# Kernel optimization log

Measured on AMD Instinct MI355X. Metric: run time of the kernel, lower is better.

## Reference

```python
import jax, jax.numpy as jnp
import numpy as np

P1 = np.array([[1000.0, 0.0, 128.0, 64000.0],
               [0.0, 1000.0, 128.0, 64000.0],
               [0.0, 0.0, 1.0, 500.0]])
P2 = np.array([[-128.0, 0.0, 1000.0, 64000.0],
               [-128.0, 1000.0, 0.0, 64000.0],
               [-1.0, 0.0, 0.0, 500.0]])


def calculate_fundamental_matrix(P_src, P_dst):
    # l2 = F21 @ x1 : maps a point in P_src onto a line in P_dst
    C1 = -np.linalg.inv(P_src[:3, :3]) @ P_src[:3, 3]
    e = P_dst @ np.append(C1, 1.0)          # epipole of src camera center in dst view
    return np.cross(e, np.eye(3) * -1) @ P_dst @ np.linalg.pinv(P_src)


def setup_inputs() -> dict:
    key = jax.random.key(0)
    view1 = jax.random.normal(key, (8, 4, 256, 256), dtype=jnp.float32)
    F21 = calculate_fundamental_matrix(P1, P2).astype(np.float32)
    return {"view1": view1, "F": jnp.asarray(F21)}


def reference(view1, F):
    """Epipolar image translation: out(x2) = line integral of view1 along the
    epipolar line l1 = F^T @ x2 (bilinear sampling in v, unit steps in u,
    zero outside the image). Matches fume_torch_lib.translate semantics."""
    B, C, H, W = view1.shape
    dt = view1.dtype
    F = F.astype(dt)
    ys = jnp.arange(H, dtype=dt)[:, None]   # (H,1)
    xs = jnp.arange(W, dtype=dt)[None, :]   # (1,W)
    # line coefficients l = F^T @ [x, y, 1], per output pixel -> (H,W)
    a = F[0, 0] * xs + F[1, 0] * ys + F[2, 0]
    b = F[0, 1] * xs + F[1, 1] * ys + F[2, 1]
    c = F[0, 2] * xs + F[1, 2] * ys + F[2, 2]
    n = jnp.sqrt(a * a + b * b) + jnp.asarray(1e-12, dt)
    a, b, c = a / n, b / n, c / n
    ok = (jnp.abs(b) > 1e-6).astype(dt)                 # drop near-vertical lines
    b_safe = jnp.where(jnp.abs(b) > 1e-6, b, jnp.asarray(1.0, dt))

    def step(acc, u):
        uf = u.astype(dt)
        v = -(a * uf + c) / b_safe                      # (H,W) source row per out pixel
        v0 = jnp.floor(v)
        f = v - v0
        i0 = v0.astype(jnp.int32)
        i1 = i0 + 1
        m0 = ((i0 >= 0) & (i0 < H)).astype(dt)
        m1 = ((i1 >= 0) & (i1 < H)).astype(dt)
        col = jax.lax.dynamic_index_in_dim(view1, u, axis=3, keepdims=False)  # (B,C,H)
        s0 = col[:, :, jnp.clip(i0, 0, H - 1)]          # (B,C,H,W)
        s1 = col[:, :, jnp.clip(i1, 0, H - 1)]
        val = (s0 * (1.0 - f) * m0 + s1 * f * m1) * ok
        return acc + val, None

    out, _ = jax.lax.scan(step, jnp.zeros_like(view1), jnp.arange(W))
    return out
```

## Files before the change

kernel.cpp:

```cpp
#include <hip/hip_runtime.h>
#include <cstdint>

constexpr int Hh = 256, Ww = 256, BCc = 32;
constexpr int RBLK = 35;
constexpr int USTRIDE = RBLK * BCc * 8 * 2;
constexpr int UPLANES = 264;

typedef _Float16 half2v   __attribute__((ext_vector_type(2)));
typedef _Float16 half8v   __attribute__((ext_vector_type(8)));
typedef __fp16   fp16x2   __attribute__((ext_vector_type(2)));
typedef float    float16v __attribute__((ext_vector_type(16)));
typedef uint32_t uint4v   __attribute__((ext_vector_type(4)));

static __device__ inline half2v pack2(float a, float b) {
    fp16x2 r = __builtin_amdgcn_cvt_pkrtz(a, b);
    return __builtin_bit_cast(half2v, r);
}

__global__ __launch_bounds__(256) void fume_pack(const float* __restrict__ in,
                                                 char* __restrict__ T4) {
    const int t   = threadIdx.x;
    const int bid = blockIdx.x;
    if (bid >= 512) {
        constexpr int NA = UPLANES * 3 * 32;
        constexpr int NB = 8 * 32 * 32;
        for (int id = (bid - 512) * 256 + t; id < NA + NB; id += 8 * 256) {
            int u, blk, ch;
            if (id < NA) {
                u = id / 96;
                int rem = id - u * 96;
                int bsel = rem >> 5;
                blk = (bsel == 0) ? 0 : (bsel == 1 ? 33 : 34);
                ch = rem & 31;
            } else {
                int id2 = id - NA;
                u = 256 + (id2 >> 10);
                int rem = id2 & 1023;
                blk = 1 + (rem >> 5);
                ch = rem & 31;
            }
            uint4v z = {0, 0, 0, 0};
            *(uint4v*)(T4 + (size_t)u * USTRIDE + blk * 512 + ch * 16) = z;
        }
        return;
    }
    __shared__ float lds[8][8][65];
    const int chg = bid & 3;
    const int r0  = ((bid >> 2) & 31) * 8;
    const int u0  = (bid >> 7) * 64;
    const int blk = (r0 >> 3) + 1;

#pragma unroll
    for (int it = 0; it < 16; ++it) {
        int idx = it * 256 + t;
        int ch = idx >> 9, rr = (idx >> 6) & 7, uu = idx & 63;
        lds[ch][rr][uu] =
            in[(chg * 8 + ch) * (Hh * Ww) + (r0 + rr) * Ww + u0 + uu];
    }
    __syncthreads();
    const int chl = t & 7;
#pragma unroll
    for (int p = 0; p < 2; ++p) {
        int u_l = (t >> 3) + p * 32;
        uint32_t w[4];
#pragma unroll
        for (int j = 0; j < 4; ++j) {
            half2v pr = pack2(lds[chl][2 * j][u_l], lds[chl][2 * j + 1][u_l]);
            __builtin_memcpy(&w[j], &pr, 4);
        }
        uint4v val = {w[0], w[1], w[2], w[3]};
        *(uint4v*)(T4 + (size_t)(u0 + u_l) * USTRIDE + blk * 512
                   + (chg * 8 + chl) * 16) = val;
    }
}

__global__ __launch_bounds__(256, 4) void fume_mfma(const char* __restrict__ T4,
                                                    const float* __restrict__ Fm,
                                                    float* __restrict__ out) {
    __shared__ float red[4][32][33];
    const int t    = threadIdx.x;
    const int lane = t & 63;
    const int wq   = t >> 6;
    const int px   = lane & 31;
    const int h    = lane >> 5;
    const int x0   = ((int)blockIdx.x & 7) * 32;
    const int y    = (int)blockIdx.x >> 3;
    const int x    = x0 + px;

    float xf = (float)x, yf = (float)y;
    float a = Fm[0] * xf + Fm[3] * yf + Fm[6];
    float b = Fm[1] * xf + Fm[4] * yf + Fm[7];
    float c = Fm[2] * xf + Fm[5] * yf + Fm[8];
    float n = sqrtf(a * a + b * b) + 1e-12f;
    a /= n; b /= n; c /= n;

    float alpha, beta_i;
    int u_lo, u_hi;
    if (fabsf(b) > 1e-6f) {
        alpha  = -a / b;
        beta_i = -c / b + 8.f;
        u_lo = 0; u_hi = Ww - 1;
        if (fabsf(alpha) > 1e-12f) {
            float inv = 1.f / alpha;
            float t0 = (7.f - beta_i) * inv;
            float t1 = (264.f - beta_i) * inv;
            int lo = (int)floorf(fminf(t0, t1));
            int hi = (int)ceilf (fmaxf(t0, t1));
            u_lo = lo > 0 ? lo : 0;
            u_hi = hi < (Ww - 1) ? hi : (Ww - 1);
        } else if (beta_i <= 7.f || beta_i >= 264.f) {
            u_lo = 1 << 20; u_hi = -(1 << 20);
        }
    } else {
        alpha = 0.f; beta_i = 3.0e4f;
        u_lo = 1 << 20; u_hi = -(1 << 20);
    }

    float xA = (float)x0, xB = (float)(x0 + 31);
    float aA = Fm[0] * xA + Fm[3] * yf + Fm[6];
    float bA = Fm[1] * xA + Fm[4] * yf + Fm[7];
    float cA = Fm[2] * xA + Fm[5] * yf + Fm[8];
    float aB = Fm[0] * xB + Fm[3] * yf + Fm[6];
    float bB = Fm[1] * xB + Fm[4] * yf + Fm[7];
    float cB = Fm[2] * xB + Fm[5] * yf + Fm[8];
    float alA = -aA / bA, beA = -cA / bA + 8.f;
    float alB = -aB / bB, beB = -cB / bB + 8.f;

    int lo = u_lo, hi = u_hi;
#pragma unroll
    for (int off = 1; off < 64; off <<= 1) {
        int l2 = __shfl_xor(lo, off, 64);
        int h2 = __shfl_xor(hi, off, 64);
        lo = lo < l2 ? lo : l2;
        hi = hi > h2 ? hi : h2;
    }
    lo = __builtin_amdgcn_readfirstlane(lo);
    hi = __builtin_amdgcn_readfirstlane(hi);

    float16v acc = {0.f, 0.f, 0.f, 0.f, 0.f, 0.f, 0.f, 0.f,
                    0.f, 0.f, 0.f, 0.f, 0.f, 0.f, 0.f, 0.f};

    if (lo <= hi) {
        int len = hi - lo + 1;
        int C   = (len + 3) >> 2;
        int cq  = (C + 3) >> 2;
        int nit = C - wq * cq;
        nit = nit < 0 ? 0 : (nit > cq ? cq : nit);
        int us  = lo + wq * cq * 4;

        float uf  = (float)(us + lane);
        float vAl = fmaf(alA, uf, beA);
        float vBl = fmaf(alB, uf, beB);
        float mnu = fminf(vAl, vBl);
        float Mf  = floorf(fmaf(mnu, 0.125f, -0.125f));
        Mf = fmaxf(0.f, fminf(Mf, 33.f));
        int   vMo  = (int)Mf << 9;
        float vB8f = Mf * 8.f;
        int   vB8i = __builtin_bit_cast(int, vB8f);

        float v   = fmaf(alpha, (float)us, beta_i);
        float l8h = (float)(8 * h);
        const char* pb  = T4 + (size_t)us * USTRIDE;
        const int voff  = (h << 9) + (px << 4);

        const half2v one2  = {(_Float16)1.f, (_Float16)1.f};
        const half2v zero2 = {(_Float16)0.f, (_Float16)0.f};

        uint4v bA4[4], bB4[4], bC4[4];

#define FUME_ISS(BUF, BASE)                                                   \
    do {                                                                      \
        _Pragma("unroll")                                                     \
        for (int i_ = 0; i_ < 4; ++i_) {                                      \
            int idx_ = (BASE) + i_;                                           \
            int Mo_  = __builtin_amdgcn_readlane(vMo, idx_);                  \
            (BUF)[i_] = *(const uint4v*)(pb + (size_t)idx_ * USTRIDE          \
                                         + (size_t)Mo_ + voff);               \
        }                                                                     \
    } while (0)

#define FUME_COMP(BUF, BASE)                                                  \
    do {                                                                      \
        _Pragma("unroll")                                                     \
        for (int i_ = 0; i_ < 4; ++i_) {                                      \
            int idx_ = (BASE) + i_;                                           \
            float b8_ = __builtin_bit_cast(                                   \
                float, __builtin_amdgcn_readlane(vB8i, idx_));                \
            float vbl_ = (v - b8_) - l8h;                                     \
            half2v vb2_ = pack2(vbl_, vbl_);                                  \
            uint32_t aw_[4];                                                  \
            _Pragma("unroll")                                                 \
            for (int j_ = 0; j_ < 4; ++j_) {                                  \
                half2v cj_ = {(_Float16)(float)(2 * j_),                      \
                              (_Float16)(float)(2 * j_ + 1)};                 \
                half2v d_  = vb2_ - cj_;                                      \
                half2v ad_ = __builtin_elementwise_abs(d_);                   \
                half2v tj_ = __builtin_elementwise_max(one2 - ad_, zero2);    \
                __builtin_memcpy(&aw_[j_], &tj_, 4);                          \
            }                                                                 \
            half8v A_;                                                        \
            __builtin_memcpy(&A_, aw_, 16);                                   \
            half8v B_ = __builtin_bit_cast(half8v, (BUF)[i_]);                \
            acc = __builtin_amdgcn_mfma_f32_32x32x16_f16(A_, B_, acc, 0, 0, 0);\
            v += alpha;                                                       \
        }                                                                     \
    } while (0)

        if (nit > 0) {
            FUME_ISS(bA4, 0);
            if (nit > 1) FUME_ISS(bB4, 4);
            int cc = 0;
            for (;;) {
                if (cc + 2 < nit) FUME_ISS(bC4, (cc + 2) * 4);
                FUME_COMP(bA4, cc * 4);
                if (++cc >= nit) break;
                if (cc + 2 < nit) FUME_ISS(bA4, (cc + 2) * 4);
                FUME_COMP(bB4, cc * 4);
                if (++cc >= nit) break;
                if (cc + 2 < nit) FUME_ISS(bB4, (cc + 2) * 4);
                FUME_COMP(bC4, cc * 4);
                if (++cc >= nit) break;
            }
        }
#undef FUME_ISS
#undef FUME_COMP
    }

#pragma unroll
    for (int r = 0; r < 16; ++r) {
        int m = (r & 3) + 8 * (r >> 2) + 4 * h;
        red[wq][m][px] = acc[r];
    }
    __syncthreads();
    {
        int pxs = t & 31, cg = t >> 5;
#pragma unroll
        for (int jj = 0; jj < 4; ++jj) {
            int ch = cg + 8 * jj;
            float val = red[0][pxs][ch] + red[1][pxs][ch]
                      + red[2][pxs][ch] + red[3][pxs][ch];
            out[(size_t)ch * (Hh * Ww) + y * Ww + x0 + pxs] = val;
        }
    }
}

__global__ __launch_bounds__(256) void fume_fallback(const float* __restrict__ src,
                                                     const float* __restrict__ Fm,
                                                     float* __restrict__ out) {
    int g = blockIdx.x * 256 + threadIdx.x;
    int part = g & 3;
    int pix  = g >> 2;
    int x = pix & (Ww - 1);
    int y = pix >> 8;
    int ch0 = part * 8;
    float xf = (float)x, yf = (float)y;
    float a = Fm[0] * xf + Fm[3] * yf + Fm[6];
    float b = Fm[1] * xf + Fm[4] * yf + Fm[7];
    float c = Fm[2] * xf + Fm[5] * yf + Fm[8];
    float n = sqrtf(a * a + b * b) + 1e-12f;
    a /= n; b /= n; c /= n;
    float acc[8];
#pragma unroll
    for (int k = 0; k < 8; ++k) acc[k] = 0.f;
    if (fabsf(b) > 1e-6f) {
        float alpha = -a / b, beta = -c / b;
        for (int u = 0; u < Ww; ++u) {
            float v  = fmaf(alpha, (float)u, beta);
            float rf = floorf(v);
            float f  = v - rf;
            int   ri = (int)rf;
            float w0 = ((unsigned)ri       < (unsigned)Hh) ? (1.f - f) : 0.f;
            float w1 = ((unsigned)(ri + 1) < (unsigned)Hh) ? f         : 0.f;
            int r0 = ri < 0 ? 0 : (ri > Hh - 1 ? Hh - 1 : ri);
            int r1 = ri + 1 < 0 ? 0 : (ri + 1 > Hh - 1 ? Hh - 1 : ri + 1);
#pragma unroll
            for (int k = 0; k < 8; ++k) {
                float s0 = src[(size_t)(ch0 + k) * (Hh * Ww) + r0 * Ww + u];
                float s1 = src[(size_t)(ch0 + k) * (Hh * Ww) + r1 * Ww + u];
                acc[k] = fmaf(w0, s0, fmaf(w1, s1, acc[k]));
            }
        }
    }
#pragma unroll
    for (int k = 0; k < 8; ++k)
        out[(size_t)(ch0 + k) * (Hh * Ww) + pix] = acc[k];
}

extern "C" void kernel_launch(void* const* d_in, const int* in_sizes, int n_in,
                              void* d_out, int out_size, void* d_ws, size_t ws_size,
                              hipStream_t stream) {
    const float* view1 = (const float*)d_in[0];
    const float* Fm    = (const float*)d_in[1];
    float* out = (float*)d_out;

    constexpr size_t t4_bytes = (size_t)UPLANES * USTRIDE;
    if (ws_size >= t4_bytes) {
        char* T4 = (char*)d_ws;
        fume_pack<<<520, 256, 0, stream>>>(view1, T4);
        fume_mfma<<<2048, 256, 0, stream>>>(T4, Fm, out);
    } else {
        fume_fallback<<<(Hh * Ww * 4) / 256, 256, 0, stream>>>(view1, Fm, out);
    }
}
```

Baseline: 97.55 us.

## Remap block order, shrink prefetch to double buffer, fuse tent weight ops

Reorders the block-to-pixel mapping so that consecutive blocks cover interleaved rows instead of adjacent x tiles, which changes which blocks run together and their cache locality. Replaces the triple-buffered gather pipeline with a double-buffered one. The last iteration issues a redundant clamped prefetch so the loop needs no branches. The tent weights are computed with a bitmask abs and a clamped packed add instead of abs plus max, and the per-lane row offset is folded ahead of the loop. Less prefetch depth lowers register use but can expose more memory latency.

```diff
diff --git a/kernel.cpp b/kernel.cpp
--- a/kernel.cpp
+++ b/kernel.cpp
@@ -83,8 +83,10 @@
     const int wq   = t >> 6;
     const int px   = lane & 31;
     const int h    = lane >> 5;
-    const int x0   = ((int)blockIdx.x & 7) * 32;
-    const int y    = (int)blockIdx.x >> 3;
+    const int bid  = (int)blockIdx.x;
+    const int idx8 = bid >> 3;
+    const int y    = ((bid & 7) << 5) + (idx8 >> 3);
+    const int x0   = (idx8 & 7) * 32;
     const int x    = x0 + px;
 
     float xf = (float)x, yf = (float)y;
@@ -158,35 +160,36 @@
         float vB8f = Mf * 8.f;
         int   vB8i = __builtin_bit_cast(int, vB8f);
 
-        float v   = fmaf(alpha, (float)us, beta_i);
         float l8h = (float)(8 * h);
+        float vh  = fmaf(alpha, (float)us, beta_i) - l8h;
         const char* pb  = T4 + (size_t)us * USTRIDE;
         const int voff  = (h << 9) + (px << 4);
 
-        const half2v one2  = {(_Float16)1.f, (_Float16)1.f};
-        const half2v zero2 = {(_Float16)0.f, (_Float16)0.f};
-
-        uint4v bA4[4], bB4[4], bC4[4];
-
-#define FUME_ISS(BUF, BASE)                                                   \
+        const half2v one2 = {(_Float16)1.f, (_Float16)1.f};
+
+        uint4v b0[4], b1[4];
+
+#define FUME_ISS(BUF, CH)                                                     \
     do {                                                                      \
+        const int base_ = (CH) * 4;                                           \
         _Pragma("unroll")                                                     \
         for (int i_ = 0; i_ < 4; ++i_) {                                      \
-            int idx_ = (BASE) + i_;                                           \
+            int idx_ = base_ + i_;                                            \
             int Mo_  = __builtin_amdgcn_readlane(vMo, idx_);                  \
             (BUF)[i_] = *(const uint4v*)(pb + (size_t)idx_ * USTRIDE          \
                                          + (size_t)Mo_ + voff);               \
         }                                                                     \
     } while (0)
 
-#define FUME_COMP(BUF, BASE)                                                  \
+#define FUME_COMP(BUF, CH)                                                    \
     do {                                                                      \
+        const int base_ = (CH) * 4;                                           \
         _Pragma("unroll")                                                     \
         for (int i_ = 0; i_ < 4; ++i_) {                                      \
-            int idx_ = (BASE) + i_;                                           \
+            int idx_ = base_ + i_;                                            \
             float b8_ = __builtin_bit_cast(                                   \
                 float, __builtin_amdgcn_readlane(vB8i, idx_));                \
-            float vbl_ = (v - b8_) - l8h;                                     \
+            float vbl_ = vh - b8_;                                            \
             half2v vb2_ = pack2(vbl_, vbl_);                                  \
             uint32_t aw_[4];                                                  \
             _Pragma("unroll")                                                 \
@@ -194,33 +197,37 @@
                 half2v cj_ = {(_Float16)(float)(2 * j_),                      \
                               (_Float16)(float)(2 * j_ + 1)};                 \
                 half2v d_  = vb2_ - cj_;                                      \
-                half2v ad_ = __builtin_elementwise_abs(d_);                   \
-                half2v tj_ = __builtin_elementwise_max(one2 - ad_, zero2);    \
+                uint32_t du_;                                                 \
+                __builtin_memcpy(&du_, &d_, 4);                               \
+                du_ &= 0x7fff7fffu;                                           \
+                half2v ad_;                                                   \
+                __builtin_memcpy(&ad_, &du_, 4);                              \
+                half2v tj_;                                                   \
+                asm("v_pk_add_f16 %0, %1, %2 neg_lo:[0,1] neg_hi:[0,1] clamp" \
+                    : "=v"(tj_)                                               \
+                    : "v"(one2), "v"(ad_));                                   \
                 __builtin_memcpy(&aw_[j_], &tj_, 4);                          \
             }                                                                 \
             half8v A_;                                                        \
             __builtin_memcpy(&A_, aw_, 16);                                   \
             half8v B_ = __builtin_bit_cast(half8v, (BUF)[i_]);                \
             acc = __builtin_amdgcn_mfma_f32_32x32x16_f16(A_, B_, acc, 0, 0, 0);\
-            v += alpha;                                                       \
+            vh += alpha;                                                      \
         }                                                                     \
     } while (0)
 
         if (nit > 0) {
-            FUME_ISS(bA4, 0);
-            if (nit > 1) FUME_ISS(bB4, 4);
+            FUME_ISS(b0, 0);
             int cc = 0;
-            for (;;) {
-                if (cc + 2 < nit) FUME_ISS(bC4, (cc + 2) * 4);
-                FUME_COMP(bA4, cc * 4);
-                if (++cc >= nit) break;
-                if (cc + 2 < nit) FUME_ISS(bA4, (cc + 2) * 4);
-                FUME_COMP(bB4, cc * 4);
-                if (++cc >= nit) break;
-                if (cc + 2 < nit) FUME_ISS(bB4, (cc + 2) * 4);
-                FUME_COMP(bC4, cc * 4);
-                if (++cc >= nit) break;
+            while (cc + 2 <= nit) {
+                FUME_ISS(b1, cc + 1);
+                FUME_COMP(b0, cc);
+                int pf = (cc + 2 < nit) ? cc + 2 : nit - 1;
+                FUME_ISS(b0, pf);
+                FUME_COMP(b1, cc + 1);
+                cc += 2;
             }
+            if (cc < nit) FUME_COMP(b0, cc);
         }
 #undef FUME_ISS
 #undef FUME_COMP
```

Measured after the change: 93.60 us. -4.1%, faster.
